# Kernel optimization log

Measured on AMD Instinct MI355X. Metric: run time of the kernel, lower is better.

Reference implementation:

```python
import jax, jax.numpy as jnp
import numpy as np

T, B, D, H, C = 512, 128, 256, 512, 10


def setup_inputs() -> dict:
    key = jax.random.key(0)
    ks = jax.random.split(key, 3)
    init_Whx = np.sqrt(6.0 / (H + D)).astype(np.float32)
    init_Whh = np.sqrt(6.0 / (H + H)).astype(np.float32)
    x = jax.random.normal(ks[0], (T, B, D), dtype=jnp.float32)
    W_hx = jax.random.uniform(ks[1], (D, H), dtype=jnp.float32, minval=-init_Whx, maxval=init_Whx)
    W_hh = jax.random.uniform(ks[2], (H, H), dtype=jnp.float32, minval=-init_Whh, maxval=init_Whh)
    W_ph = jnp.zeros((H, C), dtype=jnp.float32)
    b_h = jnp.zeros((H,), dtype=jnp.float32)
    b_p = jnp.zeros((C,), dtype=jnp.float32)
    return {"x": x, "W_hx": W_hx, "W_hh": W_hh, "W_ph": W_ph, "b_h": b_h, "b_p": b_p}


def reference(x, W_hx, W_hh, W_ph, b_h, b_p):
    # x: [T, B, D]. Sequential tanh recurrence over T via lax.scan.
    h0 = jnp.zeros((x.shape[1], W_hh.shape[0]), dtype=x.dtype)

    def step(h, x_t):
        h_new = jnp.tanh(x_t @ W_hx + h @ W_hh + b_h)
        return h_new, None

    h_final, _ = jax.lax.scan(step, h0, x)
    # Original detaches state before the output projection.
    h_final = jax.lax.stop_gradient(h_final)
    return h_final @ W_ph + b_p
```

## Files before the change

kernel.cpp:

```cpp
#include <hip/hip_runtime.h>
#include <cstdint>
#include <cstddef>

#define T_ 512
#define B_ 128
#define D_ 256
#define H_ 512
#define C_ 10

typedef float  f32x4 __attribute__((ext_vector_type(4)));
typedef short  s16x8 __attribute__((ext_vector_type(8)));
typedef _Float16 v8h  __attribute__((ext_vector_type(8)));
typedef unsigned u32x8 __attribute__((ext_vector_type(8)));

static __device__ __forceinline__ unsigned short f2bf(float f) {
    unsigned u = __builtin_bit_cast(unsigned, f);
    unsigned r = u + 0x7FFFu + ((u >> 16) & 1u);
    return (unsigned short)(r >> 16);
}

static __device__ __forceinline__ unsigned char f2e4m3_sw(float f) {
    unsigned u = __builtin_bit_cast(unsigned, f);
    unsigned sgn = (u >> 24) & 0x80u;
    float a = fabsf(f);
    if (a != a) return (unsigned char)(sgn | 0x7E);
    if (a >= 448.0f) return (unsigned char)(sgn | 0x7E);
    if (a < 0.015625f) {
        int qv = (int)rintf(a * 512.0f);
        if (qv > 7) return (unsigned char)(sgn | 0x08);
        return (unsigned char)(sgn | qv);
    }
    unsigned ub = __builtin_bit_cast(unsigned, a);
    unsigned rr = ub + 0x7FFFFu + ((ub >> 20) & 1u);
    int E = (int)(rr >> 23) - 127 + 7;
    unsigned m = (rr >> 20) & 7u;
    if (E < 1)  { E = 0; m = 7; }
    if (E > 15) { E = 15; m = 6; }
    if (E == 15 && m == 7) m = 6;
    return (unsigned char)(sgn | ((unsigned)E << 3) | m);
}
template <bool HI>
static __device__ __forceinline__ unsigned cvt2_fp8(float a, float b, unsigned old) {
#if __has_builtin(__builtin_amdgcn_cvt_pk_fp8_f32)
    return (unsigned)__builtin_amdgcn_cvt_pk_fp8_f32(a, b, (int)old, HI);
#else
    unsigned p = (unsigned)f2e4m3_sw(a) | ((unsigned)f2e4m3_sw(b) << 8);
    return HI ? ((old & 0x0000FFFFu) | (p << 16)) : ((old & 0xFFFF0000u) | p);
#endif
}

static __device__ __forceinline__ float tanh_f(float x) {
    float ex = __expf(2.0f * x);
    return 1.0f - 2.0f * __builtin_amdgcn_rcpf(ex + 1.0f);
}


__global__ void k_whxT(const float* __restrict__ Whx, unsigned short* __restrict__ WhxT) {
    int idx = blockIdx.x * 256 + threadIdx.x;
    int n = idx >> 8;
    int k = idx & 255;
    WhxT[n * 256 + k] = f2bf(Whx[k * 512 + n]);
}

__global__ void k_wfrag8(const float* __restrict__ Whh, unsigned char* __restrict__ Wf8) {
    int gid = blockIdx.x * 256 + threadIdx.x;
    int l = gid & 63, grp = gid >> 6;
    int nb = grp & 7, s = (grp >> 3) & 3, Wt = grp >> 5;
    int col = 128 * Wt + 16 * nb + (l & 15);
    int qa = l >> 4;
    unsigned dw[8];
#pragma unroll
    for (int d = 0; d < 8; ++d) {
        float vv[4];
#pragma unroll
        for (int b = 0; b < 4; ++b) {
            int j = d * 4 + b;
            int c = 128 * s + 64 * (j >> 4) + 16 * (j & 3) + 4 * ((j >> 2) & 3) + qa;
            vv[b] = Whh[(size_t)c * 512 + col];
        }
        unsigned p = cvt2_fp8<false>(vv[0], vv[1], 0u);
        dw[d] = cvt2_fp8<true>(vv[2], vv[3], p);
    }
    u32x8 out;
#pragma unroll
    for (int d = 0; d < 8; ++d) out[d] = dw[d];
    *((u32x8*)Wf8 + gid) = out;
}

__global__ void __launch_bounds__(256) k_gemm1(const float* __restrict__ x,
                                               const unsigned short* __restrict__ WhxT,
                                               const float* __restrict__ bh,
                                               char* __restrict__ Zr) {
    __shared__ char smem[32768];
    unsigned short* Asm = (unsigned short*)smem;
    unsigned short* Bsm = (unsigned short*)(smem + 8192);

    const int tid = threadIdx.x;
    const int bid = blockIdx.x;
    const int nt = bid & 3, mt = bid >> 2;
    const int r0 = mt * 128, n0 = nt * 128;
    const int w  = tid >> 6, l = tid & 63;
    const int wm = (w >> 1) * 64, wn = (w & 1) * 64;
    const int lr = l & 15, lk = (l >> 4) * 8;

    const int arow = tid >> 2, akc = (tid & 3) * 8;
    const int bcol = tid >> 1, bkc = (tid & 1) * 16;

    f32x4 acc[4][4] = {};

    for (int kk = 0; kk < 256; kk += 32) {
#pragma unroll
        for (int half = 0; half < 2; ++half) {
            const int r = arow + half * 64;
            const float* ap = x + (size_t)(r0 + r) * 256 + kk + akc;
            float4 f0 = *(const float4*)ap;
            float4 f1 = *(const float4*)(ap + 4);
            uint4 av;
            av.x = (unsigned)f2bf(f0.x) | ((unsigned)f2bf(f0.y) << 16);
            av.y = (unsigned)f2bf(f0.z) | ((unsigned)f2bf(f0.w) << 16);
            av.z = (unsigned)f2bf(f1.x) | ((unsigned)f2bf(f1.y) << 16);
            av.w = (unsigned)f2bf(f1.z) | ((unsigned)f2bf(f1.w) << 16);
            *(uint4*)&Asm[r * 32 + akc] = av;
        }
        const unsigned short* bsrc = WhxT + (size_t)(n0 + bcol) * 256 + kk + bkc;
        uint4 bv0 = *(const uint4*)bsrc;
        uint4 bv1 = *(const uint4*)(bsrc + 8);
        *(uint4*)&Bsm[bcol * 32 + bkc] = bv0;
        *(uint4*)&Bsm[bcol * 32 + bkc + 8] = bv1;
        __syncthreads();

        s16x8 af[4], bf[4];
#pragma unroll
        for (int mi = 0; mi < 4; ++mi)
            af[mi] = *(const s16x8*)&Asm[(wm + mi * 16 + lr) * 32 + lk];
#pragma unroll
        for (int ni = 0; ni < 4; ++ni)
            bf[ni] = *(const s16x8*)&Bsm[(wn + ni * 16 + lr) * 32 + lk];
#pragma unroll
        for (int mi = 0; mi < 4; ++mi)
#pragma unroll
            for (int ni = 0; ni < 4; ++ni)
                acc[mi][ni] = __builtin_amdgcn_mfma_f32_16x16x32_bf16(af[mi], bf[ni], acc[mi][ni], 0, 0, 0);
        __syncthreads();
    }

    _Float16* Szr = (_Float16*)smem;
#pragma unroll
    for (int mi = 0; mi < 4; ++mi)
#pragma unroll
        for (int ni = 0; ni < 4; ++ni) {
            const int col_l = wn + ni * 16 + lr;
            const float bhv = bh[n0 + col_l];
            const int g   = (col_l >> 5) & 3;
            const int qhi = ((col_l >> 4) & 1) * 4;
#pragma unroll
            for (int e = 0; e < 4; ++e) {
                const int b   = wm + mi * 16 + (l >> 4) * 4 + e;
                const int cu  = b >> 4;
                const int m_r = ((b & 15) >> 2) * 16 + lr;
                Szr[((cu * 4 + g) * 64 + m_r) * 8 + qhi + e] = (_Float16)(acc[mi][ni][e] + bhv);
            }
        }
    __syncthreads();
    {
        const uint4* srcv = (const uint4*)smem;
#pragma unroll
        for (int i = 0; i < 8; ++i) {
            const int o   = tid * 128 + i * 16;
            const int cuo = o >> 12;
            char* dst = Zr + ((size_t)((mt * 8 + cuo) * 4 + nt)) * 4096 + (o & 4095);
            *(uint4*)dst = srcv[o >> 4];
        }
    }
}

#define MM128(C_, A_, B_) \
    asm("v_mfma_f32_16x16x128_f8f6f4 %0, %1, %2, %0" : "+v"(C_) : "v"(A_), "a"(B_))

__global__
__attribute__((amdgpu_flat_work_group_size(512, 512), amdgpu_waves_per_eu(2, 2)))
void k_rnn(const unsigned char* __restrict__ Wf8,
           const char* __restrict__ Zr,
           float* __restrict__ hf) {
    __shared__ char hA[2][8192];

    const int tid = threadIdx.x, cu = blockIdx.x;
    const int w8 = tid >> 6;
    const int W  = w8 >> 1;
    const int hf4 = w8 & 1;
    const int l = tid & 63;
    const int r = l & 15, q = l >> 4;

    u32x8 BA[4][4];
    {
        const u32x8* Wb = (const u32x8*)Wf8;
#pragma unroll
        for (int s = 0; s < 4; ++s)
#pragma unroll
            for (int jn = 0; jn < 4; ++jn)
                BA[s][jn] = Wb[(size_t)(((W * 4 + s) * 8) + 4 * hf4 + jn) * 64 + l];
    }

    ((uint4*)hA)[tid]       = uint4{0, 0, 0, 0};
    ((uint4*)hA)[512 + tid] = uint4{0, 0, 0, 0};
    __syncthreads();

    const int qa = r & 3, rq = r >> 2;
    int rdo[4][2];
#pragma unroll
    for (int s = 0; s < 4; ++s) {
        rdo[s][0] = s * 2048 + q * 512 + ((r ^ q) << 4);
        rdo[s][1] = rdo[s][0] + 256;
    }
    int wd[4];
#pragma unroll
    for (int e = 0; e < 4; ++e)
        wd[e] = W * 2048 + qa * 512 + hf4 * 256 + (((4 * q + e) ^ qa) << 4) + 4 * rq;

    const char* zp = Zr + ((size_t)cu * 4 + W) * 4096 + (size_t)(2 * hf4) * 1024 + (size_t)l * 16;
    v8h zl0 = *(const v8h*)zp;
    v8h zl1 = *(const v8h*)(zp + 1024);

    for (int t = 0; t < T_; ++t) {
        char* rb = &hA[t & 1][0];
        char* ob = &hA[(t & 1) ^ 1][0];

        u32x8 av[4];
#pragma unroll
        for (int s = 0; s < 4; ++s) {
            uint4 lo = *(const uint4*)(rb + rdo[s][0]);
            uint4 hi = *(const uint4*)(rb + rdo[s][1]);
            av[s][0] = lo.x; av[s][1] = lo.y; av[s][2] = lo.z; av[s][3] = lo.w;
            av[s][4] = hi.x; av[s][5] = hi.y; av[s][6] = hi.z; av[s][7] = hi.w;
        }

        const char* zq = (t + 1 < T_) ? zp + 131072 : zp;
        v8h zn0 = *(const v8h*)zq;
        v8h zn1 = *(const v8h*)(zq + 1024);
        zp = zq;

        f32x4 cc[4];
#pragma unroll
        for (int jn = 0; jn < 4; ++jn) cc[jn] = f32x4{0.f, 0.f, 0.f, 0.f};

#pragma unroll
        for (int s = 0; s < 4; ++s)
#pragma unroll
            for (int jn = 0; jn < 4; ++jn)
                MM128(cc[jn], av[s], BA[s][jn]);

        __builtin_amdgcn_sched_barrier(0);
        asm volatile("s_nop 7\n\ts_nop 7\n\ts_nop 7\n\ts_nop 7\n\ts_nop 7\n\ts_nop 7" ::);
        __builtin_amdgcn_sched_barrier(0);

#pragma unroll
        for (int e = 0; e < 4; ++e) {
            float h0 = tanh_f(cc[0][e] + (float)zl0[e]);
            float h1 = tanh_f(cc[1][e] + (float)zl0[4 + e]);
            float h2 = tanh_f(cc[2][e] + (float)zl1[e]);
            float h3 = tanh_f(cc[3][e] + (float)zl1[4 + e]);
            unsigned p = cvt2_fp8<false>(h0, h1, 0u);
            p = cvt2_fp8<true>(h2, h3, p);
            *(unsigned*)(ob + wd[e]) = p;
            if (t == T_ - 1) {
                size_t row = (size_t)(16 * cu + 4 * q + e) * 512 + 128 * W + 64 * hf4 + r;
                hf[row + 0]  = h0; hf[row + 16] = h1;
                hf[row + 32] = h2; hf[row + 48] = h3;
            }
        }
        zl0 = zn0; zl1 = zn1;
        __syncthreads();
    }
}

__global__ void k_out(const float* __restrict__ hf, const float* __restrict__ Wph,
                      const float* __restrict__ bp, float* __restrict__ out) {
    __shared__ float red[160];
    int b = blockIdx.x, t = threadIdx.x;
    if (t < 160) {
        int c = t >> 4, ks = (t & 15) * 32;
        float s = 0.f;
        for (int u = 0; u < 32; ++u)
            s += hf[b * H_ + ks + u] * Wph[(ks + u) * C_ + c];
        red[t] = s;
    }
    __syncthreads();
    if (t < C_) {
        float s = bp[t];
        for (int i = 0; i < 16; ++i) s += red[t * 16 + i];
        out[b * C_ + t] = s;
    }
}

extern "C" void kernel_launch(void* const* d_in, const int* in_sizes, int n_in,
                              void* d_out, int out_size, void* d_ws, size_t ws_size,
                              hipStream_t stream) {
    const float* x   = (const float*)d_in[0];
    const float* Whx = (const float*)d_in[1];
    const float* Whh = (const float*)d_in[2];
    const float* Wph = (const float*)d_in[3];
    const float* bh  = (const float*)d_in[4];
    const float* bp  = (const float*)d_in[5];
    float* out = (float*)d_out;

    char* ws = (char*)d_ws;
    unsigned short* WhxT = (unsigned short*)(ws);
    unsigned char*  Wf8  = (unsigned char*)(ws + 262144);
    char*           Zr   = ws + 786432;
    float*          hf   = (float*)(ws + 786432 + 67108864);

    hipLaunchKernelGGL(k_whxT,   dim3(512),  dim3(256), 0, stream, Whx, WhxT);
    hipLaunchKernelGGL(k_wfrag8, dim3(32),   dim3(256), 0, stream, Whh, Wf8);
    hipLaunchKernelGGL(k_gemm1,  dim3(2048), dim3(256), 0, stream, x, WhxT, bh, Zr);
    hipLaunchKernelGGL(k_rnn,    dim3(8),    dim3(512), 0, stream, Wf8, Zr, hf);
    hipLaunchKernelGGL(k_out,    dim3(128),  dim3(256), 0, stream, hf, Wph, bp, out);
}
```

Before: 660.0 us.

## Seed MFMA accumulators with input projection and stagger tanh epilogue per column block

Accumulators now start from the precomputed input-projection term, so the bias add after the MFMA chain goes away. The MFMA chains are reordered to finish one output column block at a time. The tanh and fp8 pack work is split into stages separated by fixed nop walls, so each stage can start once its block's MFMA chain has drained instead of waiting behind one long wall. This is meant to shorten the serial per-timestep critical path of the recurrence. In exchange it uses split 16-bit LDS stores and relies on hand-tuned nop counts to cover MFMA result hazards.

```diff
diff --git a/kernel.cpp b/kernel.cpp
--- a/kernel.cpp
+++ b/kernel.cpp
@@ -176,6 +176,11 @@
 
 #define MM128(C_, A_, B_) \
     asm("v_mfma_f32_16x16x128_f8f6f4 %0, %1, %2, %0" : "+v"(C_) : "v"(A_), "a"(B_))
+#define SB0() __builtin_amdgcn_sched_barrier(0)
+#define WALL48() do { SB0(); \
+    asm volatile("s_nop 7\n\ts_nop 7\n\ts_nop 7\n\ts_nop 7\n\ts_nop 7\n\ts_nop 7" ::); \
+    SB0(); } while (0)
+#define WALL16() do { SB0(); asm volatile("s_nop 7\n\ts_nop 7" ::); SB0(); } while (0)
 
 __global__
 __attribute__((amdgpu_flat_work_group_size(512, 512), amdgpu_waves_per_eu(2, 2)))
@@ -239,35 +244,61 @@
         v8h zn1 = *(const v8h*)(zq + 1024);
         zp = zq;
 
-        f32x4 cc[4];
-#pragma unroll
-        for (int jn = 0; jn < 4; ++jn) cc[jn] = f32x4{0.f, 0.f, 0.f, 0.f};
-
-#pragma unroll
-        for (int s = 0; s < 4; ++s)
-#pragma unroll
-            for (int jn = 0; jn < 4; ++jn)
-                MM128(cc[jn], av[s], BA[s][jn]);
-
-        __builtin_amdgcn_sched_barrier(0);
-        asm volatile("s_nop 7\n\ts_nop 7\n\ts_nop 7\n\ts_nop 7\n\ts_nop 7\n\ts_nop 7" ::);
-        __builtin_amdgcn_sched_barrier(0);
-
+        f32x4 cc0, cc1, cc2, cc3;
+#pragma unroll
+        for (int e = 0; e < 4; ++e) cc0[e] = (float)zl0[e];
+        MM128(cc0, av[0], BA[0][0]); MM128(cc0, av[1], BA[1][0]);
+        MM128(cc0, av[2], BA[2][0]); MM128(cc0, av[3], BA[3][0]);
+        SB0();
+#pragma unroll
+        for (int e = 0; e < 4; ++e) cc1[e] = (float)zl0[4 + e];
+        MM128(cc1, av[0], BA[0][1]); MM128(cc1, av[1], BA[1][1]);
+        MM128(cc1, av[2], BA[2][1]); MM128(cc1, av[3], BA[3][1]);
+        SB0();
+#pragma unroll
+        for (int e = 0; e < 4; ++e) cc2[e] = (float)zl1[e];
+        MM128(cc2, av[0], BA[0][2]); MM128(cc2, av[1], BA[1][2]);
+        MM128(cc2, av[2], BA[2][2]); MM128(cc2, av[3], BA[3][2]);
+        SB0();
+#pragma unroll
+        for (int e = 0; e < 4; ++e) cc3[e] = (float)zl1[4 + e];
+        MM128(cc3, av[0], BA[0][3]); MM128(cc3, av[1], BA[1][3]);
+        MM128(cc3, av[2], BA[2][3]); MM128(cc3, av[3], BA[3][3]);
+
+        WALL48();
+        float h0[4];
+#pragma unroll
+        for (int e = 0; e < 4; ++e) h0[e] = tanh_f(cc0[e]);
+
+        WALL16();
 #pragma unroll
         for (int e = 0; e < 4; ++e) {
-            float h0 = tanh_f(cc[0][e] + (float)zl0[e]);
-            float h1 = tanh_f(cc[1][e] + (float)zl0[4 + e]);
-            float h2 = tanh_f(cc[2][e] + (float)zl1[e]);
-            float h3 = tanh_f(cc[3][e] + (float)zl1[4 + e]);
-            unsigned p = cvt2_fp8<false>(h0, h1, 0u);
-            p = cvt2_fp8<true>(h2, h3, p);
-            *(unsigned*)(ob + wd[e]) = p;
+            float h1 = tanh_f(cc1[e]);
+            unsigned p = cvt2_fp8<false>(h0[e], h1, 0u);
+            *(unsigned short*)(ob + wd[e]) = (unsigned short)p;
             if (t == T_ - 1) {
                 size_t row = (size_t)(16 * cu + 4 * q + e) * 512 + 128 * W + 64 * hf4 + r;
-                hf[row + 0]  = h0; hf[row + 16] = h1;
-                hf[row + 32] = h2; hf[row + 48] = h3;
+                hf[row + 0]  = h0[e]; hf[row + 16] = h1;
             }
         }
+
+        WALL16();
+        float h2[4];
+#pragma unroll
+        for (int e = 0; e < 4; ++e) h2[e] = tanh_f(cc2[e]);
+
+        WALL16();
+#pragma unroll
+        for (int e = 0; e < 4; ++e) {
+            float h3 = tanh_f(cc3[e]);
+            unsigned p = cvt2_fp8<false>(h2[e], h3, 0u);
+            *(unsigned short*)(ob + wd[e] + 2) = (unsigned short)p;
+            if (t == T_ - 1) {
+                size_t row = (size_t)(16 * cu + 4 * q + e) * 512 + 128 * W + 64 * hf4 + r;
+                hf[row + 32] = h2[e]; hf[row + 48] = h3;
+            }
+        }
+
         zl0 = zn0; zl1 = zn1;
         __syncthreads();
     }
```

Measured after the change: 704.9 us. 1.07x slower.
